# Performance work log

Measured on AMD Instinct MI355X. Metric: run time of the kernel, lower is better.

Reference implementation:

```python
import jax, jax.numpy as jnp
import numpy as np

N, E, B = 20000, 320000, 128      # nodes, edges, graphs in batch
H = 32                            # h_atom == n_bond
N_ATOM_FEAT, N_BOND_FEAT = 64, 16
N_LAYERS = 2


def setup_inputs() -> dict:
    key = jax.random.key(0)
    ks = jax.random.split(key, 12)
    s = 0.1
    return dict(
        n_feat=jax.random.normal(ks[0], (N, N_ATOM_FEAT), jnp.float32),
        e_feat=jax.random.normal(ks[1], (E, N_BOND_FEAT), jnp.float32),
        src=jax.random.randint(ks[2], (E,), 0, N, jnp.int32),
        dst=jax.random.randint(ks[3], (E,), 0, N, jnp.int32),
        graph_ids=jnp.sort(jax.random.randint(ks[4], (N,), 0, B, jnp.int32)),
        W_atom=jax.random.normal(ks[5], (N_ATOM_FEAT, H), jnp.float32) * s,
        b_atom=jnp.zeros((H,), jnp.float32),
        W_bond=jax.random.normal(ks[6], (N_BOND_FEAT, H), jnp.float32) * s,
        b_bond=jnp.zeros((H,), jnp.float32),
        W_e1=jax.random.normal(ks[7], (H, H), jnp.float32) * s,
        b_e1=jnp.zeros((H,), jnp.float32),
        W_e2=jax.random.normal(ks[8], (H, H * H), jnp.float32) * s,
        b_e2=jnp.zeros((H * H,), jnp.float32),
        W_ih=jax.random.normal(ks[9], (3 * H, H), jnp.float32) * s,
        W_hh=jax.random.normal(ks[10], (3 * H, H), jnp.float32) * s,
        b_ih=jnp.zeros((3 * H,), jnp.float32),
        b_hh=jnp.zeros((3 * H,), jnp.float32),
    )


def _gru_step(x, h, W_ih, W_hh, b_ih, b_hh):
    # torch nn.GRU single-cell update (seq_len=1)
    gi = x @ W_ih.T + b_ih
    gh = h @ W_hh.T + b_hh
    ir, iz, ig = jnp.split(gi, 3, axis=-1)
    hr, hz, hg = jnp.split(gh, 3, axis=-1)
    r = jax.nn.sigmoid(ir + hr)
    z = jax.nn.sigmoid(iz + hz)
    n = jnp.tanh(ig + r * hg)
    return (1.0 - z) * n + z * h


def reference(n_feat, e_feat, src, dst, graph_ids, W_atom, b_atom, W_bond, b_bond,
              W_e1, b_e1, W_e2, b_e2, W_ih, W_hh, b_ih, b_hh):
    # dense embeddings
    h = n_feat @ W_atom + b_atom              # [N, H]
    h_bond = e_feat @ W_bond + b_bond         # [E, H]
    # NNConv edge network -> per-edge weight matrix [E, H_in, H_out]
    ew = jax.nn.relu(h_bond @ W_e1 + b_e1) @ W_e2 + b_e2
    W_edge = ew.reshape(E, H, H)
    # in-degree for mean aggregation (zero in-degree -> 0, like DGL mean)
    deg = jax.ops.segment_sum(jnp.ones((E,), h.dtype), dst, num_segments=N)
    inv_deg = 1.0 / jnp.maximum(deg, 1.0)
    for _ in range(N_LAYERS):
        msg = jnp.einsum('ei,eio->eo', h[src], W_edge)                  # [E, H]
        agg = jax.ops.segment_sum(msg, dst, num_segments=N) * inv_deg[:, None]
        m = jax.nn.relu(agg)
        h = _gru_step(m, h, W_ih, W_hh, b_ih, b_hh)
    # dgl.mean_nodes: per-graph mean of node states
    gsum = jax.ops.segment_sum(h, graph_ids, num_segments=B)            # [B, H]
    gcnt = jax.ops.segment_sum(jnp.ones((N,), h.dtype), graph_ids, num_segments=B)
    return gsum / jnp.maximum(gcnt, 1.0)[:, None]
```

## Files before the change

kernel.cpp:

```cpp
#include <hip/hip_runtime.h>
#include <hip/hip_fp16.h>
#include <math.h>

#define N_NODES 20000
#define N_EDGES 320000
#define NB 128
#define H 32
#define AF 64
#define BF 16
#define SCB 79
#define SCP 20224
#define EMB_BLOCKS 2500
#define PACK_BLOCKS 66
#define ZERO_BLOCKS 16

typedef _Float16 f16x2 __attribute__((ext_vector_type(2)));

__device__ __forceinline__ float fast_sigmoid(float x) {
  return 1.0f / (1.0f + __expf(-x));
}
__device__ __forceinline__ float fast_tanh(float x) {
  float e2 = __expf(2.0f * x);
  return 1.0f - 2.0f / (e2 + 1.0f);
}
__device__ __forceinline__ unsigned int pk2(float a, float b) {
  union { f16x2 h; unsigned int u; } p;
  p.h[0] = (_Float16)a;
  p.h[1] = (_Float16)b;
  return p.u;
}
__device__ __forceinline__ float uph(unsigned int u, int hi) {
  union { unsigned int u; f16x2 h; } x; x.u = u;
  return hi ? (float)x.h[1] : (float)x.h[0];
}
__device__ __forceinline__ float dot2(unsigned int a, unsigned int b, float c) {
  union { unsigned int u; f16x2 h; } ua, ub;
  ua.u = a; ub.u = b;
#if __has_builtin(__builtin_amdgcn_fdot2)
  return __builtin_amdgcn_fdot2(ua.h, ub.h, c, false);
#else
  return c + (float)ua.h[0] * (float)ub.h[0] + (float)ua.h[1] * (float)ub.h[1];
#endif
}

__global__ __launch_bounds__(256) void prep(const float* __restrict__ nf,
    const float* __restrict__ W, const float* __restrict__ b, float* __restrict__ h,
    const float* __restrict__ We2, const float* __restrict__ be2,
    unsigned int* __restrict__ Wp, int* __restrict__ hist2buf) {
  int blk = blockIdx.x;
  int tid = threadIdx.x;
  if (blk < EMB_BLOCKS) {
    __shared__ float Ws[AF * H];
    __shared__ float nfs[8][AF];
    for (int v = tid; v < AF * H; v += 256) Ws[v] = W[v];
    int n0 = blk * 8;
    for (int v = tid; v < 8 * AF; v += 256) {
      int nl = v / AF, k = v % AF;
      nfs[nl][k] = nf[(size_t)(n0 + nl) * AF + k];
    }
    __syncthreads();
    int nl = tid / H, o = tid % H;
    int n = n0 + nl;
    float acc = b[o];
#pragma unroll
    for (int k = 0; k < AF; k++) acc += nfs[nl][k] * Ws[k * H + o];
    h[(size_t)n * H + o] = acc;
  } else if (blk < EMB_BLOCKS + PACK_BLOCKS) {
    int idx = (blk - EMB_BLOCKS) * 256 + tid;
    if (idx < 33 * 512) {
      int j = idx >> 9, r = idx & 511;
      int ip = r >> 5, o = r & 31;
      const float* src = (j < 32) ? (We2 + (size_t)j * (H * H)) : be2;
      Wp[idx] = pk2(src[(2 * ip) * H + o], src[(2 * ip + 1) * H + o]);
    }
  } else {
    int idx = (blk - EMB_BLOCKS - PACK_BLOCKS) * 256 + tid;
    for (int i = idx; i < 2 * N_NODES; i += ZERO_BLOCKS * 256) hist2buf[i] = 0;
  }
}

__global__ void hist2(const int* __restrict__ src, const int* __restrict__ dst,
                      int* __restrict__ hsrc, int* __restrict__ hdst) {
  int e = blockIdx.x * 256 + threadIdx.x;
  if (e < N_EDGES) {
    atomicAdd(&hsrc[src[e]], 1);
    atomicAdd(&hdst[dst[e]], 1);
  }
}

__global__ __launch_bounds__(256) void scan_partial(const int* __restrict__ hist_s,
    const int* __restrict__ hist_d, int* __restrict__ part, int* __restrict__ bsum) {
  __shared__ int wsums[4];
  int which = blockIdx.y;
  const int* __restrict__ hh = which ? hist_d : hist_s;
  int i = blockIdx.x * 256 + threadIdx.x;
  int v = (i < N_NODES) ? hh[i] : 0;
  int lane = threadIdx.x & 63, wid = threadIdx.x >> 6;
  int incl = v;
#pragma unroll
  for (int off = 1; off < 64; off <<= 1) {
    int t = __shfl_up(incl, off, 64);
    if (lane >= off) incl += t;
  }
  if (lane == 63) wsums[wid] = incl;
  __syncthreads();
  int woff = 0;
#pragma unroll
  for (int w = 0; w < 4; w++) if (w < wid) woff += wsums[w];
  part[which * SCP + i] = woff + incl - v;
  if (threadIdx.x == 0)
    bsum[which * SCB + blockIdx.x] = wsums[0] + wsums[1] + wsums[2] + wsums[3];
}

__global__ __launch_bounds__(256) void scan_tops(int* __restrict__ bsum,
    const int* __restrict__ gid, int* __restrict__ gstart) {
  __shared__ int s[2 * SCB];
  int tid = threadIdx.x;
  if (tid < 2 * SCB) s[tid] = bsum[tid];
  if (tid < NB) {
    int g = tid;
    int lo = 0, hi = N_NODES;
    while (lo < hi) { int mid = (lo + hi) >> 1; if (gid[mid] < g) lo = mid + 1; else hi = mid; }
    gstart[g] = lo;
    if (g == 0) gstart[NB] = N_NODES;
  }
  __syncthreads();
  if (tid < 2) {
    int run = 0;
    for (int b = 0; b < SCB; b++) { int t = s[tid * SCB + b]; s[tid * SCB + b] = run; run += t; }
  }
  __syncthreads();
  if (tid < 2 * SCB) bsum[tid] = s[tid];
}

__global__ __launch_bounds__(256) void scan_final(const int* __restrict__ part,
    const int* __restrict__ bsum, const int* __restrict__ hist_d,
    int* __restrict__ cur_s, int* __restrict__ cur_d,
    int* __restrict__ seg_s, int* __restrict__ seg_d, float* __restrict__ inv_deg) {
  int which = blockIdx.y;
  int i = blockIdx.x * 256 + threadIdx.x;
  if (i >= N_NODES) return;
  int ex = part[which * SCP + i] + bsum[which * SCB + blockIdx.x];
  if (which == 0) {
    cur_s[i] = ex; seg_s[i] = ex;
    if (i == 0) seg_s[N_NODES] = N_EDGES;
  } else {
    cur_d[i] = ex; seg_d[i] = ex;
    inv_deg[i] = 1.0f / fmaxf((float)hist_d[i], 1.0f);
    if (i == 0) seg_d[N_NODES] = N_EDGES;
  }
}

__global__ void scatter2_fast(const int* __restrict__ src, const int* __restrict__ dst,
    int* __restrict__ cur_s, int* __restrict__ cur_d,
    int* __restrict__ pos_s, int* __restrict__ dpos) {
  int e = blockIdx.x * 256 + threadIdx.x;
  if (e >= N_EDGES) return;
  int s = src[e], d = dst[e];
  int ps = atomicAdd(&cur_s[s], 1);
  int pd = atomicAdd(&cur_d[d], 1);
  dpos[ps] = pd;
  pos_s[e] = ps;
}

__global__ void scatter2_full(const int* __restrict__ src, const int* __restrict__ dst,
    int* __restrict__ cur_s, int* __restrict__ cur_d,
    int* __restrict__ src_s, int* __restrict__ dst_s,
    int* __restrict__ pos_s, int* __restrict__ dpos) {
  int e = blockIdx.x * 256 + threadIdx.x;
  if (e >= N_EDGES) return;
  int s = src[e], d = dst[e];
  int ps = atomicAdd(&cur_s[s], 1);
  int pd = atomicAdd(&cur_d[d], 1);
  src_s[ps] = s;
  dst_s[ps] = d;
  dpos[ps] = pd;
  pos_s[e] = ps;
}

__global__ __launch_bounds__(256) void edge_r(const float* __restrict__ ef,
    const float* __restrict__ Wb, const float* __restrict__ bb,
    const float* __restrict__ We1, const float* __restrict__ be1,
    const int* __restrict__ pos_s, unsigned int* __restrict__ rh) {
  __shared__ float Wbs[BF * H];
  __shared__ unsigned int W1p[16 * H];
  __shared__ float efs[32 * 20];
  __shared__ unsigned int hbp[32 * 20];
  int tid = threadIdx.x;
  for (int v = tid; v < BF * H; v += 256) Wbs[v] = Wb[v];
  for (int v = tid; v < 16 * H; v += 256) {
    int jp = v >> 5, o = v & 31;
    W1p[v] = pk2(We1[(2 * jp) * H + o], We1[(2 * jp + 1) * H + o]);
  }
  int e0 = blockIdx.x * 32;
  if (tid < 128) {
    float4 d = ((const float4*)(ef + (size_t)e0 * BF))[tid];
    ((float4*)(efs + (tid >> 2) * 20))[tid & 3] = d;
  }
  __syncthreads();
  int el = tid >> 3, oq = tid & 7;
  const float4* Wb4 = (const float4*)Wbs;
  const float4* efv = (const float4*)(efs + el * 20);
  float4 hb = ((const float4*)bb)[oq];
#pragma unroll
  for (int kq = 0; kq < 4; kq++) {
    float4 e4 = efv[kq];
    float4 w;
    w = Wb4[(kq * 4 + 0) * 8 + oq];
    hb.x += e4.x * w.x; hb.y += e4.x * w.y; hb.z += e4.x * w.z; hb.w += e4.x * w.w;
    w = Wb4[(kq * 4 + 1) * 8 + oq];
    hb.x += e4.y * w.x; hb.y += e4.y * w.y; hb.z += e4.y * w.z; hb.w += e4.y * w.w;
    w = Wb4[(kq * 4 + 2) * 8 + oq];
    hb.x += e4.z * w.x; hb.y += e4.z * w.y; hb.z += e4.z * w.z; hb.w += e4.z * w.w;
    w = Wb4[(kq * 4 + 3) * 8 + oq];
    hb.x += e4.w * w.x; hb.y += e4.w * w.y; hb.z += e4.w * w.z; hb.w += e4.w * w.w;
  }
  ((uint2*)(hbp + el * 20))[oq] = make_uint2(pk2(hb.x, hb.y), pk2(hb.z, hb.w));
  __syncthreads();
  float4 acc = ((const float4*)be1)[oq];
  const uint4* hb4 = (const uint4*)(hbp + el * 20);
#pragma unroll
  for (int q = 0; q < 4; q++) {
    uint4 hp = hb4[q];
    uint4 w;
    w = ((const uint4*)(W1p + (4 * q + 0) * H))[oq];
    acc.x = dot2(hp.x, w.x, acc.x); acc.y = dot2(hp.x, w.y, acc.y);
    acc.z = dot2(hp.x, w.z, acc.z); acc.w = dot2(hp.x, w.w, acc.w);
    w = ((const uint4*)(W1p + (4 * q + 1) * H))[oq];
    acc.x = dot2(hp.y, w.x, acc.x); acc.y = dot2(hp.y, w.y, acc.y);
    acc.z = dot2(hp.y, w.z, acc.z); acc.w = dot2(hp.y, w.w, acc.w);
    w = ((const uint4*)(W1p + (4 * q + 2) * H))[oq];
    acc.x = dot2(hp.z, w.x, acc.x); acc.y = dot2(hp.z, w.y, acc.y);
    acc.z = dot2(hp.z, w.z, acc.z); acc.w = dot2(hp.z, w.w, acc.w);
    w = ((const uint4*)(W1p + (4 * q + 3) * H))[oq];
    acc.x = dot2(hp.w, w.x, acc.x); acc.y = dot2(hp.w, w.y, acc.y);
    acc.z = dot2(hp.w, w.z, acc.z); acc.w = dot2(hp.w, w.w, acc.w);
  }
  acc.x = fmaxf(acc.x, 0.0f); acc.y = fmaxf(acc.y, 0.0f);
  acc.z = fmaxf(acc.z, 0.0f); acc.w = fmaxf(acc.w, 0.0f);
  int ps = pos_s[e0 + el];
  uint2 st;
  st.x = pk2(acc.x, acc.y);
  st.y = pk2(acc.z, acc.w);
  ((uint2*)(rh + (size_t)ps * 16))[oq] = st;
}

__global__ __launch_bounds__(256) void edge_msg_T(const float* __restrict__ h,
    const unsigned int* __restrict__ Wp, const unsigned int* __restrict__ rh,
    const int* __restrict__ seg_s, const int* __restrict__ dpos,
    unsigned int* __restrict__ msg_h) {
  __shared__ unsigned int Ts[8 * 512];
  __shared__ unsigned int hp[8 * 16];
  __shared__ float hb[8 * H];
  __shared__ int sseg[9];
  int tid = threadIdx.x;
  int n0 = blockIdx.x * 8;
  if (tid < 128) {
    int nl = tid >> 4, ip = tid & 15;
    float2 hv = ((const float2*)(h + (size_t)(n0 + nl) * H))[ip];
    hp[nl * 16 + ip] = pk2(hv.x, hv.y);
  }
  if (tid < 9) sseg[tid] = seg_s[n0 + tid];
  __syncthreads();
  {
    int jp = tid >> 4, oh = tid & 15;
    uint2 w0[16], w1[16];
    const unsigned int* W0 = Wp + (size_t)(2 * jp) * 512 + 2 * oh;
    const unsigned int* W1 = Wp + (size_t)(2 * jp + 1) * 512 + 2 * oh;
#pragma unroll
    for (int ip = 0; ip < 16; ip++) {
      w0[ip] = *(const uint2*)(W0 + ip * 32);
      w1[ip] = *(const uint2*)(W1 + ip * 32);
    }
#pragma unroll
    for (int nl = 0; nl < 8; nl++) {
      uint4 h0 = ((const uint4*)(hp + nl * 16))[0];
      uint4 h1 = ((const uint4*)(hp + nl * 16))[1];
      uint4 h2 = ((const uint4*)(hp + nl * 16))[2];
      uint4 h3 = ((const uint4*)(hp + nl * 16))[3];
      unsigned int hr[16] = {h0.x, h0.y, h0.z, h0.w, h1.x, h1.y, h1.z, h1.w,
                             h2.x, h2.y, h2.z, h2.w, h3.x, h3.y, h3.z, h3.w};
      float t00 = 0.f, t01 = 0.f, t10 = 0.f, t11 = 0.f;
#pragma unroll
      for (int ip = 0; ip < 16; ip++) {
        unsigned int hpv = hr[ip];
        t00 = dot2(hpv, w0[ip].x, t00);
        t01 = dot2(hpv, w0[ip].y, t01);
        t10 = dot2(hpv, w1[ip].x, t10);
        t11 = dot2(hpv, w1[ip].y, t11);
      }
      ((uint2*)(Ts + nl * 512 + jp * 32 + 2 * oh))[0] =
          make_uint2(pk2(t00, t10), pk2(t01, t11));
    }
  }
  {
    int nl = tid >> 5, o = tid & 31;
    const unsigned int* Wb32 = Wp + (size_t)32 * 512 + o;
    float acc = 0.f;
#pragma unroll
    for (int ip = 0; ip < 16; ip++)
      acc = dot2(hp[nl * 16 + ip], Wb32[ip * 32], acc);
    hb[nl * H + o] = acc;
  }
  __syncthreads();
  int lane = tid & 63, wid = tid >> 6;
  int el = lane >> 3, t = lane & 7;
  for (int s = 0; s < 8; s++) {
    int a = sseg[s], bnd = sseg[s + 1];
    int ww = (wid + s) & 3;
    if (a + ww * 8 >= bnd) continue;
    const unsigned int* Trow = Ts + s * 512;
    uint4 tw[16];
#pragma unroll
    for (int jp = 0; jp < 16; jp++) tw[jp] = ((const uint4*)(Trow + jp * 32))[t];
    float4 hbv = ((const float4*)(hb + s * H))[t];
    for (int base = a + ww * 8; base < bnd; base += 32) {
      int e = base + el;
      bool valid = (e < bnd);
      int pd = 0;
      unsigned int rr[16];
#pragma unroll
      for (int k = 0; k < 16; k++) rr[k] = 0u;
      if (valid) {
        pd = dpos[e];
        const uint4* rp = (const uint4*)(rh + (size_t)e * 16);
        *(uint4*)(&rr[0])  = rp[0];
        *(uint4*)(&rr[4])  = rp[1];
        *(uint4*)(&rr[8])  = rp[2];
        *(uint4*)(&rr[12]) = rp[3];
      }
      float4 acc = hbv;
#pragma unroll
      for (int jp = 0; jp < 16; jp++) {
        unsigned int rj = rr[jp];
        uint4 w = tw[jp];
        acc.x = dot2(rj, w.x, acc.x);
        acc.y = dot2(rj, w.y, acc.y);
        acc.z = dot2(rj, w.z, acc.z);
        acc.w = dot2(rj, w.w, acc.w);
      }
      if (valid) {
        uint2 st;
        st.x = pk2(acc.x, acc.y);
        st.y = pk2(acc.z, acc.w);
        ((uint2*)(msg_h + (size_t)pd * 16))[t] = st;
      }
    }
  }
}

__global__ __launch_bounds__(256) void compute_T_fused(const float* __restrict__ h,
    const unsigned int* __restrict__ Wp,
    unsigned int* __restrict__ Th, float* __restrict__ hbias) {
  __shared__ unsigned int Wall[9 * 512];
  __shared__ unsigned int hp[32 * 17];
  int tid = threadIdx.x;
  int n0 = blockIdx.x * 32;
  int jb = blockIdx.y;
  int nslice = (jb == 3) ? 9 : 8;
  const uint4* Wsrc = (const uint4*)(Wp + (size_t)jb * 8 * 512);
#pragma unroll
  for (int v = 0; v < 4; v++) ((uint4*)Wall)[tid + v * 256] = Wsrc[tid + v * 256];
  if (jb == 3 && tid < 128)
    ((uint4*)(Wall + 8 * 512))[tid] = ((const uint4*)(Wp + 32 * 512))[tid];
  for (int v = tid; v < 512; v += 256) {
    int nl = v >> 4, ip = v & 15;
    float2 hv = ((const float2*)(h + (size_t)(n0 + nl) * H))[ip];
    hp[nl * 17 + ip] = pk2(hv.x, hv.y);
  }
  __syncthreads();
  int nl = tid >> 3, oq = tid & 7;
  unsigned int hreg[16];
#pragma unroll
  for (int ip = 0; ip < 16; ip++) hreg[ip] = hp[nl * 17 + ip];
  int n = n0 + nl;
  float4 pacc = make_float4(0.f, 0.f, 0.f, 0.f);
  for (int jj = 0; jj < nslice; jj++) {
    const uint4* W4 = (const uint4*)(Wall + jj * 512);
    float4 acc = make_float4(0.f, 0.f, 0.f, 0.f);
#pragma unroll
    for (int ip = 0; ip < 16; ip++) {
      unsigned int hpv = hreg[ip];
      uint4 w = W4[ip * 8 + oq];
      acc.x = dot2(hpv, w.x, acc.x);
      acc.y = dot2(hpv, w.y, acc.y);
      acc.z = dot2(hpv, w.z, acc.z);
      acc.w = dot2(hpv, w.w, acc.w);
    }
    int j = jb * 8 + jj;
    if (j < H) {
      if (jj & 1) {
        uint4 st;
        st.x = pk2(pacc.x, acc.x);
        st.y = pk2(pacc.y, acc.y);
        st.z = pk2(pacc.z, acc.z);
        st.w = pk2(pacc.w, acc.w);
        ((uint4*)(Th + (size_t)n * 512 + (j >> 1) * 32))[oq] = st;
      } else {
        pacc = acc;
      }
    } else {
      ((float4*)(hbias + (size_t)n * H))[oq] = acc;
    }
  }
}

__global__ __launch_bounds__(256) void edge_msg_atomic(const unsigned int* __restrict__ rh,
    const unsigned int* __restrict__ Th, const float* __restrict__ hbias,
    const int* __restrict__ src_s, const int* __restrict__ dst_s,
    float* __restrict__ agg) {
  int tid = threadIdx.x;
  int e0 = blockIdx.x * 32;
  int el = tid >> 3, t = tid & 7;
  int e = e0 + el;
  int s = src_s[e], d = dst_s[e];
  uint2 ru2 = ((const uint2*)(rh + (size_t)e * 16))[t];
  float4 acc = ((const float4*)(hbias + (size_t)s * H))[t];
  const unsigned int* Trow = Th + (size_t)s * 512;
#pragma unroll
  for (int jp = 0; jp < 16; jp++) {
    unsigned int mine = (jp & 1) ? ru2.y : ru2.x;
    unsigned int rj = (unsigned int)__shfl((int)mine, jp >> 1, 8);
    uint4 tw = ((const uint4*)(Trow + jp * 32))[t];
    acc.x = dot2(rj, tw.x, acc.x);
    acc.y = dot2(rj, tw.y, acc.y);
    acc.z = dot2(rj, tw.z, acc.z);
    acc.w = dot2(rj, tw.w, acc.w);
  }
  float* ap = agg + (size_t)d * H + t * 4;
  atomicAdd(ap + 0, acc.x);
  atomicAdd(ap + 1, acc.y);
  atomicAdd(ap + 2, acc.z);
  atomicAdd(ap + 3, acc.w);
}

__global__ __launch_bounds__(256) void seg_gru(const unsigned int* __restrict__ msg_h,
    const int* __restrict__ seg_d, const float* __restrict__ invdeg,
    const float* __restrict__ Wih, const float* __restrict__ Whh,
    const float* __restrict__ bih, const float* __restrict__ bhh,
    float* __restrict__ h) {
  __shared__ unsigned int Wisp[96 * 18];
  __shared__ unsigned int Whsp[96 * 18];
  __shared__ unsigned int xpk[8 * 18];
  __shared__ unsigned int hpk[8 * 18];
  int tid = threadIdx.x;
  for (int v = tid; v < 96 * 16; v += 256) {
    int k = v >> 4, ip = v & 15;
    float2 wi = ((const float2*)Wih)[v];
    float2 wh = ((const float2*)Whh)[v];
    Wisp[k * 18 + ip] = pk2(wi.x, wi.y);
    Whsp[k * 18 + ip] = pk2(wh.x, wh.y);
  }
  int node = tid >> 5, o = tid & 31;
  int n = blockIdx.x * 8 + node;
  int a = seg_d[n], bseg = seg_d[n + 1];
  int q = o & 3, g = o >> 2;
  float acc[8];
#pragma unroll
  for (int k = 0; k < 8; k++) acc[k] = 0.0f;
  int nrows = bseg - a;
#pragma unroll 2
  for (int p = g; p < nrows; p += 8) {
    uint4 m = ((const uint4*)(msg_h + (size_t)(a + p) * 16))[q];
    acc[0] += uph(m.x, 0); acc[1] += uph(m.x, 1);
    acc[2] += uph(m.y, 0); acc[3] += uph(m.y, 1);
    acc[4] += uph(m.z, 0); acc[5] += uph(m.z, 1);
    acc[6] += uph(m.w, 0); acc[7] += uph(m.w, 1);
  }
#pragma unroll
  for (int k = 0; k < 8; k++) {
    acc[k] += __shfl_xor(acc[k], 4, 32);
    acc[k] += __shfl_xor(acc[k], 8, 32);
    acc[k] += __shfl_xor(acc[k], 16, 32);
  }
  float idg = invdeg[n];
  if (g == 0) {
#pragma unroll
    for (int t = 0; t < 4; t++) {
      float xa = fmaxf(acc[2 * t] * idg, 0.0f);
      float xb = fmaxf(acc[2 * t + 1] * idg, 0.0f);
      xpk[node * 18 + 4 * q + t] = pk2(xa, xb);
    }
  }
  float hval = h[(size_t)n * H + o];
  float hnb = __shfl_xor(hval, 1, 32);
  if (!(o & 1)) hpk[node * 18 + (o >> 1)] = pk2(hval, hnb);
  __syncthreads();
  float gi0 = bih[o], gi1 = bih[H + o], gi2 = bih[2 * H + o];
  float gh0 = bhh[o], gh1 = bhh[H + o], gh2 = bhh[2 * H + o];
  const uint2* xr  = (const uint2*)(xpk + node * 18);
  const uint2* hr  = (const uint2*)(hpk + node * 18);
  const uint2* wi0 = (const uint2*)(Wisp + o * 18);
  const uint2* wi1 = (const uint2*)(Wisp + (H + o) * 18);
  const uint2* wi2 = (const uint2*)(Wisp + (2 * H + o) * 18);
  const uint2* wh0 = (const uint2*)(Whsp + o * 18);
  const uint2* wh1 = (const uint2*)(Whsp + (H + o) * 18);
  const uint2* wh2 = (const uint2*)(Whsp + (2 * H + o) * 18);
#pragma unroll
  for (int t = 0; t < 8; t++) {
    uint2 xv = xr[t], hv = hr[t];
    uint2 a0 = wi0[t], a1 = wi1[t], a2 = wi2[t];
    uint2 b0 = wh0[t], b1 = wh1[t], b2 = wh2[t];
    gi0 = dot2(xv.x, a0.x, gi0); gi0 = dot2(xv.y, a0.y, gi0);
    gi1 = dot2(xv.x, a1.x, gi1); gi1 = dot2(xv.y, a1.y, gi1);
    gi2 = dot2(xv.x, a2.x, gi2); gi2 = dot2(xv.y, a2.y, gi2);
    gh0 = dot2(hv.x, b0.x, gh0); gh0 = dot2(hv.y, b0.y, gh0);
    gh1 = dot2(hv.x, b1.x, gh1); gh1 = dot2(hv.y, b1.y, gh1);
    gh2 = dot2(hv.x, b2.x, gh2); gh2 = dot2(hv.y, b2.y, gh2);
  }
  float rg = fast_sigmoid(gi0 + gh0);
  float zg = fast_sigmoid(gi1 + gh1);
  float ng = fast_tanh(gi2 + rg * gh2);
  h[(size_t)n * H + o] = (1.0f - zg) * ng + zg * hval;
}

__global__ __launch_bounds__(256) void gru_update(const float* __restrict__ agg,
    const float* __restrict__ invdeg, const float* __restrict__ Wih,
    const float* __restrict__ Whh, const float* __restrict__ bih,
    const float* __restrict__ bhh, float* __restrict__ h) {
  __shared__ float Wis[3 * H][H + 1];
  __shared__ float Whs[3 * H][H + 1];
  __shared__ float xs[8][H + 1];
  __shared__ float hsm[8][H + 1];
  int tid = threadIdx.x;
  for (int v = tid; v < 3 * H * H; v += 256) {
    int k = v / H, i = v % H;
    Wis[k][i] = Wih[v];
    Whs[k][i] = Whh[v];
  }
  int node = tid >> 5, o = tid & 31;
  int n = blockIdx.x * 8 + node;
  xs[node][o] = fmaxf(agg[(size_t)n * H + o] * invdeg[n], 0.0f);
  float hval = h[(size_t)n * H + o];
  hsm[node][o] = hval;
  __syncthreads();
  float gi0 = bih[o], gi1 = bih[H + o], gi2 = bih[2 * H + o];
  float gh0 = bhh[o], gh1 = bhh[H + o], gh2 = bhh[2 * H + o];
#pragma unroll
  for (int i = 0; i < H; i++) {
    float xi = xs[node][i], hi_ = hsm[node][i];
    gi0 += xi * Wis[o][i];
    gh0 += hi_ * Whs[o][i];
    gi1 += xi * Wis[H + o][i];
    gh1 += hi_ * Whs[H + o][i];
    gi2 += xi * Wis[2 * H + o][i];
    gh2 += hi_ * Whs[2 * H + o][i];
  }
  float rg = fast_sigmoid(gi0 + gh0);
  float zg = fast_sigmoid(gi1 + gh1);
  float ng = fast_tanh(gi2 + rg * gh2);
  h[(size_t)n * H + o] = (1.0f - zg) * ng + zg * hval;
}

__global__ __launch_bounds__(256) void readout_graph(const float* __restrict__ h,
    const int* __restrict__ gstart, float* __restrict__ out) {
  __shared__ float red[8][H + 1];
  int g = blockIdx.x;
  int a = gstart[g], b = gstart[g + 1];
  int r = threadIdx.x >> 5, o = threadIdx.x & 31;
  float s = 0.0f;
  for (int n = a + r; n < b; n += 8) s += h[(size_t)n * H + o];
  red[r][o] = s;
  __syncthreads();
  if (r == 0) {
    float t = 0.0f;
#pragma unroll
    for (int k = 0; k < 8; k++) t += red[k][o];
    out[g * H + o] = t / fmaxf((float)(b - a), 1.0f);
  }
}

extern "C" void kernel_launch(void* const* d_in, const int* in_sizes, int n_in,
                              void* d_out, int out_size, void* d_ws, size_t ws_size,
                              hipStream_t stream) {
  const float* n_feat = (const float*)d_in[0];
  const float* e_feat = (const float*)d_in[1];
  const int*   src    = (const int*)d_in[2];
  const int*   dst    = (const int*)d_in[3];
  const int*   gid    = (const int*)d_in[4];
  const float* W_atom = (const float*)d_in[5];
  const float* b_atom = (const float*)d_in[6];
  const float* W_bond = (const float*)d_in[7];
  const float* b_bond = (const float*)d_in[8];
  const float* W_e1   = (const float*)d_in[9];
  const float* b_e1   = (const float*)d_in[10];
  const float* W_e2   = (const float*)d_in[11];
  const float* b_e2   = (const float*)d_in[12];
  const float* W_ih   = (const float*)d_in[13];
  const float* W_hh   = (const float*)d_in[14];
  const float* b_ih   = (const float*)d_in[15];
  const float* b_hh   = (const float*)d_in[16];
  float* out = (float*)d_out;

  char* ws = (char*)d_ws;
  size_t off = 0;
  float*        h      = (float*)(ws + off); off += (size_t)N_NODES * H * 4;
  unsigned int* rh     = (unsigned int*)(ws + off); off += (size_t)N_EDGES * 16 * 4;
  unsigned int* Th     = (unsigned int*)(ws + off); off += (size_t)N_NODES * 512 * 4;
  float*        hbias  = (float*)(ws + off); off += (size_t)N_NODES * H * 4;
  unsigned int* Wp     = (unsigned int*)(ws + off); off += (size_t)33 * 512 * 4;
  int*   hist_s = (int*)(ws + off);   off += (size_t)N_NODES * 4;
  int*   hist_d = (int*)(ws + off);   off += (size_t)N_NODES * 4;
  int*   cur_s  = (int*)(ws + off);   off += (size_t)N_NODES * 4;
  int*   cur_d  = (int*)(ws + off);   off += (size_t)N_NODES * 4;
  int*   seg_s  = (int*)(ws + off);   off += (size_t)(N_NODES + 1) * 4;
  int*   seg_d  = (int*)(ws + off);   off += (size_t)(N_NODES + 1) * 4;
  float* invdeg = (float*)(ws + off); off += (size_t)N_NODES * 4;
  int*   part   = (int*)(ws + off);   off += (size_t)2 * SCP * 4;
  int*   bsum   = (int*)(ws + off);   off += (size_t)2 * SCB * 4;
  int*   src_s  = (int*)(ws + off);   off += (size_t)N_EDGES * 4;
  int*   dst_s  = (int*)(ws + off);   off += (size_t)N_EDGES * 4;
  int*   dpos   = (int*)(ws + off);   off += (size_t)N_EDGES * 4;
  int*   gstart = (int*)(ws + off);   off += (size_t)(NB + 1) * 4;
  float* agg    = (float*)(ws + off); off += (size_t)N_NODES * H * 4;
  unsigned int* msg_h = (unsigned int*)(ws + off); off += (size_t)N_EDGES * 16 * 4;
  int use_msg = (ws_size >= off) ? 1 : 0;
  int* pos_s = (int*)Th;

  prep<<<EMB_BLOCKS + PACK_BLOCKS + ZERO_BLOCKS, 256, 0, stream>>>(
      n_feat, W_atom, b_atom, h, W_e2, b_e2, Wp, hist_s);

  hist2<<<(N_EDGES + 255) / 256, 256, 0, stream>>>(src, dst, hist_s, hist_d);
  {
    dim3 gs(SCB, 2);
    scan_partial<<<gs, 256, 0, stream>>>(hist_s, hist_d, part, bsum);
    scan_tops<<<1, 256, 0, stream>>>(bsum, gid, gstart);
    scan_final<<<gs, 256, 0, stream>>>(part, bsum, hist_d, cur_s, cur_d,
                                       seg_s, seg_d, invdeg);
  }
  if (use_msg) {
    scatter2_fast<<<(N_EDGES + 255) / 256, 256, 0, stream>>>(src, dst, cur_s, cur_d,
                                                             pos_s, dpos);
  } else {
    scatter2_full<<<(N_EDGES + 255) / 256, 256, 0, stream>>>(src, dst, cur_s, cur_d,
                                                             src_s, dst_s, pos_s, dpos);
  }

  edge_r<<<N_EDGES / 32, 256, 0, stream>>>(e_feat, W_bond, b_bond, W_e1, b_e1,
                                           pos_s, rh);

  for (int layer = 0; layer < 2; layer++) {
    if (use_msg) {
      edge_msg_T<<<N_NODES / 8, 256, 0, stream>>>(h, Wp, rh, seg_s, dpos, msg_h);
      seg_gru<<<N_NODES / 8, 256, 0, stream>>>(msg_h, seg_d, invdeg,
                                               W_ih, W_hh, b_ih, b_hh, h);
    } else {
      dim3 gT(N_NODES / 32, 4);
      compute_T_fused<<<gT, 256, 0, stream>>>(h, Wp, Th, hbias);
      hipMemsetAsync(agg, 0, (size_t)N_NODES * H * 4, stream);
      edge_msg_atomic<<<N_EDGES / 32, 256, 0, stream>>>(rh, Th, hbias, src_s, dst_s,
                                                        agg);
      gru_update<<<N_NODES / 8, 256, 0, stream>>>(agg, invdeg,
                                                  W_ih, W_hh, b_ih, b_hh, h);
    }
  }

  readout_graph<<<NB, 256, 0, stream>>>(h, gstart, out);
}
```

Baseline: 288.5 us.

## Fuse edge scatter into edge_r and fuse layer-0 GRU with layer-1 messages

```diff
diff --git a/kernel.cpp b/kernel.cpp
--- a/kernel.cpp
+++ b/kernel.cpp
@@ -151,18 +151,6 @@
   }
 }
 
-__global__ void scatter2_fast(const int* __restrict__ src, const int* __restrict__ dst,
-    int* __restrict__ cur_s, int* __restrict__ cur_d,
-    int* __restrict__ pos_s, int* __restrict__ dpos) {
-  int e = blockIdx.x * 256 + threadIdx.x;
-  if (e >= N_EDGES) return;
-  int s = src[e], d = dst[e];
-  int ps = atomicAdd(&cur_s[s], 1);
-  int pd = atomicAdd(&cur_d[d], 1);
-  dpos[ps] = pd;
-  pos_s[e] = ps;
-}
-
 __global__ void scatter2_full(const int* __restrict__ src, const int* __restrict__ dst,
     int* __restrict__ cur_s, int* __restrict__ cur_d,
     int* __restrict__ src_s, int* __restrict__ dst_s,
@@ -178,21 +166,16 @@
   pos_s[e] = ps;
 }
 
-__global__ __launch_bounds__(256) void edge_r(const float* __restrict__ ef,
+__device__ __forceinline__ uint2 edge_r_core(const float* __restrict__ ef,
     const float* __restrict__ Wb, const float* __restrict__ bb,
     const float* __restrict__ We1, const float* __restrict__ be1,
-    const int* __restrict__ pos_s, unsigned int* __restrict__ rh) {
-  __shared__ float Wbs[BF * H];
-  __shared__ unsigned int W1p[16 * H];
-  __shared__ float efs[32 * 20];
-  __shared__ unsigned int hbp[32 * 20];
-  int tid = threadIdx.x;
+    float* Wbs, unsigned int* W1p, float* efs, unsigned int* hbp,
+    int e0, int tid) {
   for (int v = tid; v < BF * H; v += 256) Wbs[v] = Wb[v];
   for (int v = tid; v < 16 * H; v += 256) {
     int jp = v >> 5, o = v & 31;
     W1p[v] = pk2(We1[(2 * jp) * H + o], We1[(2 * jp + 1) * H + o]);
   }
-  int e0 = blockIdx.x * 32;
   if (tid < 128) {
     float4 d = ((const float4*)(ef + (size_t)e0 * BF))[tid];
     ((float4*)(efs + (tid >> 2) * 20))[tid & 3] = d;
@@ -238,30 +221,59 @@
   }
   acc.x = fmaxf(acc.x, 0.0f); acc.y = fmaxf(acc.y, 0.0f);
   acc.z = fmaxf(acc.z, 0.0f); acc.w = fmaxf(acc.w, 0.0f);
-  int ps = pos_s[e0 + el];
   uint2 st;
   st.x = pk2(acc.x, acc.y);
   st.y = pk2(acc.z, acc.w);
+  return st;
+}
+
+__global__ __launch_bounds__(256) void edge_r_scatter(const float* __restrict__ ef,
+    const float* __restrict__ Wb, const float* __restrict__ bb,
+    const float* __restrict__ We1, const float* __restrict__ be1,
+    const int* __restrict__ src, const int* __restrict__ dst,
+    int* __restrict__ cur_s, int* __restrict__ cur_d,
+    int* __restrict__ dpos, unsigned int* __restrict__ rh) {
+  __shared__ float Wbs[BF * H];
+  __shared__ unsigned int W1p[16 * H];
+  __shared__ float efs[32 * 20];
+  __shared__ unsigned int hbp[32 * 20];
+  int tid = threadIdx.x;
+  int e0 = blockIdx.x * 32;
+  uint2 st = edge_r_core(ef, Wb, bb, We1, be1, Wbs, W1p, efs, hbp, e0, tid);
+  int el = tid >> 3, oq = tid & 7;
+  int wl = tid & 63;
+  int e = e0 + el;
+  int ps = 0;
+  if (oq == 0) {
+    int s = src[e], d = dst[e];
+    ps = atomicAdd(&cur_s[s], 1);
+    int pd = atomicAdd(&cur_d[d], 1);
+    dpos[ps] = pd;
+  }
+  ps = __shfl(ps, wl & 56, 64);
   ((uint2*)(rh + (size_t)ps * 16))[oq] = st;
 }
 
-__global__ __launch_bounds__(256) void edge_msg_T(const float* __restrict__ h,
-    const unsigned int* __restrict__ Wp, const unsigned int* __restrict__ rh,
-    const int* __restrict__ seg_s, const int* __restrict__ dpos,
-    unsigned int* __restrict__ msg_h) {
-  __shared__ unsigned int Ts[8 * 512];
-  __shared__ unsigned int hp[8 * 16];
-  __shared__ float hb[8 * H];
-  __shared__ int sseg[9];
-  int tid = threadIdx.x;
-  int n0 = blockIdx.x * 8;
-  if (tid < 128) {
-    int nl = tid >> 4, ip = tid & 15;
-    float2 hv = ((const float2*)(h + (size_t)(n0 + nl) * H))[ip];
-    hp[nl * 16 + ip] = pk2(hv.x, hv.y);
-  }
-  if (tid < 9) sseg[tid] = seg_s[n0 + tid];
-  __syncthreads();
+__global__ __launch_bounds__(256) void edge_r(const float* __restrict__ ef,
+    const float* __restrict__ Wb, const float* __restrict__ bb,
+    const float* __restrict__ We1, const float* __restrict__ be1,
+    const int* __restrict__ pos_s, unsigned int* __restrict__ rh) {
+  __shared__ float Wbs[BF * H];
+  __shared__ unsigned int W1p[16 * H];
+  __shared__ float efs[32 * 20];
+  __shared__ unsigned int hbp[32 * 20];
+  int tid = threadIdx.x;
+  int e0 = blockIdx.x * 32;
+  uint2 st = edge_r_core(ef, Wb, bb, We1, be1, Wbs, W1p, efs, hbp, e0, tid);
+  int el = tid >> 3, oq = tid & 7;
+  int ps = pos_s[e0 + el];
+  ((uint2*)(rh + (size_t)ps * 16))[oq] = st;
+}
+
+__device__ __forceinline__ void msg_phase(const unsigned int* __restrict__ Wp,
+    const unsigned int* __restrict__ rh, const int* __restrict__ dpos,
+    unsigned int* __restrict__ msg_out,
+    unsigned int* Ts, const unsigned int* hp, float* hb, const int* sseg, int tid) {
   {
     int jp = tid >> 4, oh = tid & 15;
     uint2 w0[16], w1[16];
@@ -343,10 +355,207 @@
         uint2 st;
         st.x = pk2(acc.x, acc.y);
         st.y = pk2(acc.z, acc.w);
-        ((uint2*)(msg_h + (size_t)pd * 16))[t] = st;
+        ((uint2*)(msg_out + (size_t)pd * 16))[t] = st;
       }
     }
   }
+}
+
+__global__ __launch_bounds__(256) void edge_msg_T(const float* __restrict__ h,
+    const unsigned int* __restrict__ Wp, const unsigned int* __restrict__ rh,
+    const int* __restrict__ seg_s, const int* __restrict__ dpos,
+    unsigned int* __restrict__ msg_h) {
+  __shared__ unsigned int Ts[8 * 512];
+  __shared__ unsigned int hp[8 * 16];
+  __shared__ float hb[8 * H];
+  __shared__ int sseg[9];
+  int tid = threadIdx.x;
+  int n0 = blockIdx.x * 8;
+  if (tid < 128) {
+    int nl = tid >> 4, ip = tid & 15;
+    float2 hv = ((const float2*)(h + (size_t)(n0 + nl) * H))[ip];
+    hp[nl * 16 + ip] = pk2(hv.x, hv.y);
+  }
+  if (tid < 9) sseg[tid] = seg_s[n0 + tid];
+  __syncthreads();
+  msg_phase(Wp, rh, dpos, msg_h, Ts, hp, hb, sseg, tid);
+}
+
+__global__ __launch_bounds__(256) void gru_msg(const unsigned int* __restrict__ msg_in,
+    const int* __restrict__ seg_d, const float* __restrict__ invdeg,
+    const float* __restrict__ Wih, const float* __restrict__ Whh,
+    const float* __restrict__ bih, const float* __restrict__ bhh,
+    float* __restrict__ h,
+    const unsigned int* __restrict__ Wp, const unsigned int* __restrict__ rh,
+    const int* __restrict__ seg_s, const int* __restrict__ dpos,
+    unsigned int* __restrict__ msg_out) {
+  __shared__ __align__(16) char smem_u[8 * 512 * 4];
+  unsigned int* Wisp = (unsigned int*)smem_u;
+  unsigned int* Whsp = Wisp + 96 * 18;
+  unsigned int* Ts   = (unsigned int*)smem_u;
+  __shared__ unsigned int xpk[8 * 18];
+  __shared__ unsigned int hpk[8 * 18];
+  __shared__ unsigned int hp[8 * 16];
+  __shared__ float hb[8 * H];
+  __shared__ int sseg[9];
+  int tid = threadIdx.x;
+  int n0 = blockIdx.x * 8;
+  for (int v = tid; v < 96 * 16; v += 256) {
+    int k = v >> 4, ip = v & 15;
+    float2 wi = ((const float2*)Wih)[v];
+    float2 wh = ((const float2*)Whh)[v];
+    Wisp[k * 18 + ip] = pk2(wi.x, wi.y);
+    Whsp[k * 18 + ip] = pk2(wh.x, wh.y);
+  }
+  if (tid < 9) sseg[tid] = seg_s[n0 + tid];
+  int node = tid >> 5, o = tid & 31;
+  int n = n0 + node;
+  int a = seg_d[n], bseg = seg_d[n + 1];
+  int q = o & 3, g = o >> 2;
+  float acc[8];
+#pragma unroll
+  for (int k = 0; k < 8; k++) acc[k] = 0.0f;
+  int nrows = bseg - a;
+#pragma unroll 2
+  for (int p = g; p < nrows; p += 8) {
+    uint4 m = ((const uint4*)(msg_in + (size_t)(a + p) * 16))[q];
+    acc[0] += uph(m.x, 0); acc[1] += uph(m.x, 1);
+    acc[2] += uph(m.y, 0); acc[3] += uph(m.y, 1);
+    acc[4] += uph(m.z, 0); acc[5] += uph(m.z, 1);
+    acc[6] += uph(m.w, 0); acc[7] += uph(m.w, 1);
+  }
+#pragma unroll
+  for (int k = 0; k < 8; k++) {
+    acc[k] += __shfl_xor(acc[k], 4, 32);
+    acc[k] += __shfl_xor(acc[k], 8, 32);
+    acc[k] += __shfl_xor(acc[k], 16, 32);
+  }
+  float idg = invdeg[n];
+  if (g == 0) {
+#pragma unroll
+    for (int t = 0; t < 4; t++) {
+      float xa = fmaxf(acc[2 * t] * idg, 0.0f);
+      float xb = fmaxf(acc[2 * t + 1] * idg, 0.0f);
+      xpk[node * 18 + 4 * q + t] = pk2(xa, xb);
+    }
+  }
+  float hval = h[(size_t)n * H + o];
+  float hnb = __shfl_xor(hval, 1, 32);
+  if (!(o & 1)) hpk[node * 18 + (o >> 1)] = pk2(hval, hnb);
+  __syncthreads();
+  float gi0 = bih[o], gi1 = bih[H + o], gi2 = bih[2 * H + o];
+  float gh0 = bhh[o], gh1 = bhh[H + o], gh2 = bhh[2 * H + o];
+  {
+    const uint2* xr  = (const uint2*)(xpk + node * 18);
+    const uint2* hr  = (const uint2*)(hpk + node * 18);
+    const uint2* wi0 = (const uint2*)(Wisp + o * 18);
+    const uint2* wi1 = (const uint2*)(Wisp + (H + o) * 18);
+    const uint2* wi2 = (const uint2*)(Wisp + (2 * H + o) * 18);
+    const uint2* wh0 = (const uint2*)(Whsp + o * 18);
+    const uint2* wh1 = (const uint2*)(Whsp + (H + o) * 18);
+    const uint2* wh2 = (const uint2*)(Whsp + (2 * H + o) * 18);
+#pragma unroll
+    for (int t = 0; t < 8; t++) {
+      uint2 xv = xr[t], hv = hr[t];
+      uint2 a0 = wi0[t], a1 = wi1[t], a2 = wi2[t];
+      uint2 b0 = wh0[t], b1 = wh1[t], b2 = wh2[t];
+      gi0 = dot2(xv.x, a0.x, gi0); gi0 = dot2(xv.y, a0.y, gi0);
+      gi1 = dot2(xv.x, a1.x, gi1); gi1 = dot2(xv.y, a1.y, gi1);
+      gi2 = dot2(xv.x, a2.x, gi2); gi2 = dot2(xv.y, a2.y, gi2);
+      gh0 = dot2(hv.x, b0.x, gh0); gh0 = dot2(hv.y, b0.y, gh0);
+      gh1 = dot2(hv.x, b1.x, gh1); gh1 = dot2(hv.y, b1.y, gh1);
+      gh2 = dot2(hv.x, b2.x, gh2); gh2 = dot2(hv.y, b2.y, gh2);
+    }
+  }
+  float rg = fast_sigmoid(gi0 + gh0);
+  float zg = fast_sigmoid(gi1 + gh1);
+  float ng = fast_tanh(gi2 + rg * gh2);
+  float hnew = (1.0f - zg) * ng + zg * hval;
+  h[(size_t)n * H + o] = hnew;
+  float hnb2 = __shfl_xor(hnew, 1, 32);
+  if (!(o & 1)) hp[node * 16 + (o >> 1)] = pk2(hnew, hnb2);
+  __syncthreads();
+  msg_phase(Wp, rh, dpos, msg_out, Ts, hp, hb, sseg, tid);
+}
+
+__global__ __launch_bounds__(256) void seg_gru(const unsigned int* __restrict__ msg_h,
+    const int* __restrict__ seg_d, const float* __restrict__ invdeg,
+    const float* __restrict__ Wih, const float* __restrict__ Whh,
+    const float* __restrict__ bih, const float* __restrict__ bhh,
+    float* __restrict__ h) {
+  __shared__ unsigned int Wisp[96 * 18];
+  __shared__ unsigned int Whsp[96 * 18];
+  __shared__ unsigned int xpk[8 * 18];
+  __shared__ unsigned int hpk[8 * 18];
+  int tid = threadIdx.x;
+  for (int v = tid; v < 96 * 16; v += 256) {
+    int k = v >> 4, ip = v & 15;
+    float2 wi = ((const float2*)Wih)[v];
+    float2 wh = ((const float2*)Whh)[v];
+    Wisp[k * 18 + ip] = pk2(wi.x, wi.y);
+    Whsp[k * 18 + ip] = pk2(wh.x, wh.y);
+  }
+  int node = tid >> 5, o = tid & 31;
+  int n = blockIdx.x * 8 + node;
+  int a = seg_d[n], bseg = seg_d[n + 1];
+  int q = o & 3, g = o >> 2;
+  float acc[8];
+#pragma unroll
+  for (int k = 0; k < 8; k++) acc[k] = 0.0f;
+  int nrows = bseg - a;
+#pragma unroll 2
+  for (int p = g; p < nrows; p += 8) {
+    uint4 m = ((const uint4*)(msg_h + (size_t)(a + p) * 16))[q];
+    acc[0] += uph(m.x, 0); acc[1] += uph(m.x, 1);
+    acc[2] += uph(m.y, 0); acc[3] += uph(m.y, 1);
+    acc[4] += uph(m.z, 0); acc[5] += uph(m.z, 1);
+    acc[6] += uph(m.w, 0); acc[7] += uph(m.w, 1);
+  }
+#pragma unroll
+  for (int k = 0; k < 8; k++) {
+    acc[k] += __shfl_xor(acc[k], 4, 32);
+    acc[k] += __shfl_xor(acc[k], 8, 32);
+    acc[k] += __shfl_xor(acc[k], 16, 32);
+  }
+  float idg = invdeg[n];
+  if (g == 0) {
+#pragma unroll
+    for (int t = 0; t < 4; t++) {
+      float xa = fmaxf(acc[2 * t] * idg, 0.0f);
+      float xb = fmaxf(acc[2 * t + 1] * idg, 0.0f);
+      xpk[node * 18 + 4 * q + t] = pk2(xa, xb);
+    }
+  }
+  float hval = h[(size_t)n * H + o];
+  float hnb = __shfl_xor(hval, 1, 32);
+  if (!(o & 1)) hpk[node * 18 + (o >> 1)] = pk2(hval, hnb);
+  __syncthreads();
+  float gi0 = bih[o], gi1 = bih[H + o], gi2 = bih[2 * H + o];
+  float gh0 = bhh[o], gh1 = bhh[H + o], gh2 = bhh[2 * H + o];
+  const uint2* xr  = (const uint2*)(xpk + node * 18);
+  const uint2* hr  = (const uint2*)(hpk + node * 18);
+  const uint2* wi0 = (const uint2*)(Wisp + o * 18);
+  const uint2* wi1 = (const uint2*)(Wisp + (H + o) * 18);
+  const uint2* wi2 = (const uint2*)(Wisp + (2 * H + o) * 18);
+  const uint2* wh0 = (const uint2*)(Whsp + o * 18);
+  const uint2* wh1 = (const uint2*)(Whsp + (H + o) * 18);
+  const uint2* wh2 = (const uint2*)(Whsp + (2 * H + o) * 18);
+#pragma unroll
+  for (int t = 0; t < 8; t++) {
+    uint2 xv = xr[t], hv = hr[t];
+    uint2 a0 = wi0[t], a1 = wi1[t], a2 = wi2[t];
+    uint2 b0 = wh0[t], b1 = wh1[t], b2 = wh2[t];
+    gi0 = dot2(xv.x, a0.x, gi0); gi0 = dot2(xv.y, a0.y, gi0);
+    gi1 = dot2(xv.x, a1.x, gi1); gi1 = dot2(xv.y, a1.y, gi1);
+    gi2 = dot2(xv.x, a2.x, gi2); gi2 = dot2(xv.y, a2.y, gi2);
+    gh0 = dot2(hv.x, b0.x, gh0); gh0 = dot2(hv.y, b0.y, gh0);
+    gh1 = dot2(hv.x, b1.x, gh1); gh1 = dot2(hv.y, b1.y, gh1);
+    gh2 = dot2(hv.x, b2.x, gh2); gh2 = dot2(hv.y, b2.y, gh2);
+  }
+  float rg = fast_sigmoid(gi0 + gh0);
+  float zg = fast_sigmoid(gi1 + gh1);
+  float ng = fast_tanh(gi2 + rg * gh2);
+  h[(size_t)n * H + o] = (1.0f - zg) * ng + zg * hval;
 }
 
 __global__ __launch_bounds__(256) void compute_T_fused(const float* __restrict__ h,
@@ -432,86 +641,6 @@
   atomicAdd(ap + 1, acc.y);
   atomicAdd(ap + 2, acc.z);
   atomicAdd(ap + 3, acc.w);
-}
-
-__global__ __launch_bounds__(256) void seg_gru(const unsigned int* __restrict__ msg_h,
-    const int* __restrict__ seg_d, const float* __restrict__ invdeg,
-    const float* __restrict__ Wih, const float* __restrict__ Whh,
-    const float* __restrict__ bih, const float* __restrict__ bhh,
-    float* __restrict__ h) {
-  __shared__ unsigned int Wisp[96 * 18];
-  __shared__ unsigned int Whsp[96 * 18];
-  __shared__ unsigned int xpk[8 * 18];
-  __shared__ unsigned int hpk[8 * 18];
-  int tid = threadIdx.x;
-  for (int v = tid; v < 96 * 16; v += 256) {
-    int k = v >> 4, ip = v & 15;
-    float2 wi = ((const float2*)Wih)[v];
-    float2 wh = ((const float2*)Whh)[v];
-    Wisp[k * 18 + ip] = pk2(wi.x, wi.y);
-    Whsp[k * 18 + ip] = pk2(wh.x, wh.y);
-  }
-  int node = tid >> 5, o = tid & 31;
-  int n = blockIdx.x * 8 + node;
-  int a = seg_d[n], bseg = seg_d[n + 1];
-  int q = o & 3, g = o >> 2;
-  float acc[8];
-#pragma unroll
-  for (int k = 0; k < 8; k++) acc[k] = 0.0f;
-  int nrows = bseg - a;
-#pragma unroll 2
-  for (int p = g; p < nrows; p += 8) {
-    uint4 m = ((const uint4*)(msg_h + (size_t)(a + p) * 16))[q];
-    acc[0] += uph(m.x, 0); acc[1] += uph(m.x, 1);
-    acc[2] += uph(m.y, 0); acc[3] += uph(m.y, 1);
-    acc[4] += uph(m.z, 0); acc[5] += uph(m.z, 1);
-    acc[6] += uph(m.w, 0); acc[7] += uph(m.w, 1);
-  }
-#pragma unroll
-  for (int k = 0; k < 8; k++) {
-    acc[k] += __shfl_xor(acc[k], 4, 32);
-    acc[k] += __shfl_xor(acc[k], 8, 32);
-    acc[k] += __shfl_xor(acc[k], 16, 32);
-  }
-  float idg = invdeg[n];
-  if (g == 0) {
-#pragma unroll
-    for (int t = 0; t < 4; t++) {
-      float xa = fmaxf(acc[2 * t] * idg, 0.0f);
-      float xb = fmaxf(acc[2 * t + 1] * idg, 0.0f);
-      xpk[node * 18 + 4 * q + t] = pk2(xa, xb);
-    }
-  }
-  float hval = h[(size_t)n * H + o];
-  float hnb = __shfl_xor(hval, 1, 32);
-  if (!(o & 1)) hpk[node * 18 + (o >> 1)] = pk2(hval, hnb);
-  __syncthreads();
-  float gi0 = bih[o], gi1 = bih[H + o], gi2 = bih[2 * H + o];
-  float gh0 = bhh[o], gh1 = bhh[H + o], gh2 = bhh[2 * H + o];
-  const uint2* xr  = (const uint2*)(xpk + node * 18);
-  const uint2* hr  = (const uint2*)(hpk + node * 18);
-  const uint2* wi0 = (const uint2*)(Wisp + o * 18);
-  const uint2* wi1 = (const uint2*)(Wisp + (H + o) * 18);
-  const uint2* wi2 = (const uint2*)(Wisp + (2 * H + o) * 18);
-  const uint2* wh0 = (const uint2*)(Whsp + o * 18);
-  const uint2* wh1 = (const uint2*)(Whsp + (H + o) * 18);
-  const uint2* wh2 = (const uint2*)(Whsp + (2 * H + o) * 18);
-#pragma unroll
-  for (int t = 0; t < 8; t++) {
-    uint2 xv = xr[t], hv = hr[t];
-    uint2 a0 = wi0[t], a1 = wi1[t], a2 = wi2[t];
-    uint2 b0 = wh0[t], b1 = wh1[t], b2 = wh2[t];
-    gi0 = dot2(xv.x, a0.x, gi0); gi0 = dot2(xv.y, a0.y, gi0);
-    gi1 = dot2(xv.x, a1.x, gi1); gi1 = dot2(xv.y, a1.y, gi1);
-    gi2 = dot2(xv.x, a2.x, gi2); gi2 = dot2(xv.y, a2.y, gi2);
-    gh0 = dot2(hv.x, b0.x, gh0); gh0 = dot2(hv.y, b0.y, gh0);
-    gh1 = dot2(hv.x, b1.x, gh1); gh1 = dot2(hv.y, b1.y, gh1);
-    gh2 = dot2(hv.x, b2.x, gh2); gh2 = dot2(hv.y, b2.y, gh2);
-  }
-  float rg = fast_sigmoid(gi0 + gh0);
-  float zg = fast_sigmoid(gi1 + gh1);
-  float ng = fast_tanh(gi2 + rg * gh2);
-  h[(size_t)n * H + o] = (1.0f - zg) * ng + zg * hval;
 }
 
 __global__ __launch_bounds__(256) void gru_update(const float* __restrict__ agg,
@@ -613,7 +742,8 @@
   int*   dpos   = (int*)(ws + off);   off += (size_t)N_EDGES * 4;
   int*   gstart = (int*)(ws + off);   off += (size_t)(NB + 1) * 4;
   float* agg    = (float*)(ws + off); off += (size_t)N_NODES * H * 4;
-  unsigned int* msg_h = (unsigned int*)(ws + off); off += (size_t)N_EDGES * 16 * 4;
+  unsigned int* msg_h  = (unsigned int*)(ws + off); off += (size_t)N_EDGES * 16 * 4;
+  unsigned int* msg_h2 = (unsigned int*)(ws + off); off += (size_t)N_EDGES * 16 * 4;
   int use_msg = (ws_size >= off) ? 1 : 0;
   int* pos_s = (int*)Th;
 
@@ -628,23 +758,23 @@
     scan_final<<<gs, 256, 0, stream>>>(part, bsum, hist_d, cur_s, cur_d,
                                        seg_s, seg_d, invdeg);
   }
+
   if (use_msg) {
-    scatter2_fast<<<(N_EDGES + 255) / 256, 256, 0, stream>>>(src, dst, cur_s, cur_d,
-                                                             pos_s, dpos);
+    edge_r_scatter<<<N_EDGES / 32, 256, 0, stream>>>(e_feat, W_bond, b_bond,
+                                                     W_e1, b_e1, src, dst,
+                                                     cur_s, cur_d, dpos, rh);
+    edge_msg_T<<<N_NODES / 8, 256, 0, stream>>>(h, Wp, rh, seg_s, dpos, msg_h);
+    gru_msg<<<N_NODES / 8, 256, 0, stream>>>(msg_h, seg_d, invdeg,
+                                             W_ih, W_hh, b_ih, b_hh, h,
+                                             Wp, rh, seg_s, dpos, msg_h2);
+    seg_gru<<<N_NODES / 8, 256, 0, stream>>>(msg_h2, seg_d, invdeg,
+                                             W_ih, W_hh, b_ih, b_hh, h);
   } else {
     scatter2_full<<<(N_EDGES + 255) / 256, 256, 0, stream>>>(src, dst, cur_s, cur_d,
                                                              src_s, dst_s, pos_s, dpos);
-  }
-
-  edge_r<<<N_EDGES / 32, 256, 0, stream>>>(e_feat, W_bond, b_bond, W_e1, b_e1,
-                                           pos_s, rh);
-
-  for (int layer = 0; layer < 2; layer++) {
-    if (use_msg) {
-      edge_msg_T<<<N_NODES / 8, 256, 0, stream>>>(h, Wp, rh, seg_s, dpos, msg_h);
-      seg_gru<<<N_NODES / 8, 256, 0, stream>>>(msg_h, seg_d, invdeg,
-                                               W_ih, W_hh, b_ih, b_hh, h);
-    } else {
+    edge_r<<<N_EDGES / 32, 256, 0, stream>>>(e_feat, W_bond, b_bond, W_e1, b_e1,
+                                             pos_s, rh);
+    for (int layer = 0; layer < 2; layer++) {
       dim3 gT(N_NODES / 32, 4);
       compute_T_fused<<<gT, 256, 0, stream>>>(h, Wp, Th, hbias);
       hipMemsetAsync(agg, 0, (size_t)N_NODES * H * 4, stream);
```

Measured after the change: 278.9 us. 1.03x faster.
